# Performance work log

Measured on AMD Instinct MI355X. Metric: run time of the kernel, lower is better.

## Reference

```python
import jax, jax.numpy as jnp
import numpy as np
import math

B, S, D = 2, 2048, 1024
HQ, HKV = 16, 4
HD = D // HQ          # 64
N_REP = HQ // HKV     # 4
WINDOW = 256
ROPE_BASE = 10000.0


def _rope(x):
    # x: [b, s, h, hd]; interleaved-pair rotary (torchtune style)
    s, hd = x.shape[1], x.shape[-1]
    inv_freq = 1.0 / (ROPE_BASE ** (jnp.arange(0, hd, 2, dtype=jnp.float32) / hd))
    ang = jnp.arange(s, dtype=jnp.float32)[:, None] * inv_freq          # [s, hd/2]
    cos = jnp.cos(ang)[None, :, None, :].astype(x.dtype)
    sin = jnp.sin(ang)[None, :, None, :].astype(x.dtype)
    x1, x2 = x[..., ::2], x[..., 1::2]
    out = jnp.stack([x1 * cos - x2 * sin, x1 * sin + x2 * cos], axis=-1)
    return out.reshape(x.shape)


def setup_inputs() -> dict:
    key = jax.random.key(0)
    ks = jax.random.split(key, 5)
    sc = 0.02
    return {
        "x": jax.random.normal(ks[0], (B, S, D), dtype=jnp.float32),
        "Wq": jax.random.normal(ks[1], (D, HQ * HD), dtype=jnp.float32) * sc,
        "Wk": jax.random.normal(ks[2], (D, HKV * HD), dtype=jnp.float32) * sc,
        "Wv": jax.random.normal(ks[3], (D, HKV * HD), dtype=jnp.float32) * sc,
        "Wo": jax.random.normal(ks[4], (HQ * HD, D), dtype=jnp.float32) * sc,
    }


def reference(x, Wq, Wk, Wv, Wo):
    b, s, _ = x.shape
    xq = (x @ Wq).reshape(b, s, HQ, HD)
    xk = (x @ Wk).reshape(b, s, HKV, HD)
    xv = (x @ Wv).reshape(b, s, HKV, HD)

    xq = _rope(xq)
    xk = _rope(xk)

    # GQA: repeat kv heads to match query heads
    keys = jnp.repeat(xk, N_REP, axis=2)    # [b, s, HQ, HD]
    values = jnp.repeat(xv, N_REP, axis=2)

    scores = jnp.einsum("bqhd,bkhd->bhqk", xq, keys) / math.sqrt(HD)

    # symmetric sliding window: keep |i - j| <= WINDOW // 2
    idx = jnp.arange(s)
    mask = jnp.abs(idx[:, None] - idx[None, :]) <= (WINDOW // 2)  # [s, s]
    scores = jnp.where(mask[None, None], scores, -jnp.inf)

    attn = jax.nn.softmax(scores.astype(jnp.float32), axis=-1).astype(xq.dtype)
    ctx = jnp.einsum("bhqk,bkhd->bqhd", attn, values).reshape(b, s, HQ * HD)
    return ctx @ Wo
```

## Files before the change

### kernel.cpp

```cpp
#include <hip/hip_runtime.h>

typedef unsigned short u16;
typedef unsigned int u32;
typedef __attribute__((ext_vector_type(8))) short bfrag;
typedef __attribute__((ext_vector_type(4))) float f32x4;

#define S_LEN 2048
#define DMODEL 1024
#define NHQ 16
#define NHKV 4
#define HD 64
#define HALFW 128
#define ROWS 4096
#define QSCALE 0.1803368801111244f

__device__ __forceinline__ u16 f2b(float f) {
  u32 x = __float_as_uint(f);
  return (u16)((x + 0x7fffu + ((x >> 16) & 1u)) >> 16);
}

__device__ __forceinline__ u32 cvtpk(float lo, float hi) {
  u32 r;
  asm("v_cvt_pk_bf16_f32 %0, %1, %2" : "=v"(r) : "v"(lo), "v"(hi));
  return r;
}

__device__ __forceinline__ float fexp(float x) {
  float r;
  asm("v_exp_f32 %0, %1" : "=v"(r) : "v"(x));
  return r;
}

__global__ void prep_k(const float* __restrict__ x, const float* __restrict__ Wq,
                       const float* __restrict__ Wk, const float* __restrict__ Wv,
                       const float* __restrict__ Wo, u16* __restrict__ xb,
                       u16* __restrict__ Wcat_t, u16* __restrict__ Wo_t,
                       float2* __restrict__ csT) {
  __shared__ float tile[32][33];
  int y = blockIdx.y;
  int tid = threadIdx.y * 32 + threadIdx.x;
  if (y >= 88) {
    int i = (((y - 88) * 32 + blockIdx.x) * 256 + tid) * 4;
    float4 v = *reinterpret_cast<const float4*>(x + i);
    uint2 p;
    p.x = (u32)f2b(v.x) | ((u32)f2b(v.y) << 16);
    p.y = (u32)f2b(v.z) | ((u32)f2b(v.w) << 16);
    *reinterpret_cast<uint2*>(xb + i) = p;
    return;
  }
  if (y >= 80) {
    int idx = ((y - 80) * 32 + blockIdx.x) * 256 + tid;
    int s = idx >> 5, i = idx & 31;
    double inv = pow(10000.0, -(double)(2 * i) / 64.0);
    double ang = (double)s * inv;
    csT[idx] = make_float2((float)cos(ang), (float)sin(ang));
    return;
  }
  int k0 = blockIdx.x * 32;
  const float* src; u16* dst; int ncols, n0;
  if (y < 32)      { src = Wq; dst = Wcat_t;                       ncols = 1024; n0 = y * 32; }
  else if (y < 40) { src = Wk; dst = Wcat_t + (size_t)1024 * 1024; ncols = 256;  n0 = (y - 32) * 32; }
  else if (y < 48) { src = Wv; dst = Wcat_t + (size_t)1280 * 1024; ncols = 256;  n0 = (y - 40) * 32; }
  else             { src = Wo; dst = Wo_t;                         ncols = 1024; n0 = (y - 48) * 32; }
  int tx = threadIdx.x, ty = threadIdx.y;
#pragma unroll
  for (int j = 0; j < 4; ++j)
    tile[ty + 8 * j][tx] = src[(size_t)(k0 + ty + 8 * j) * ncols + n0 + tx];
  __syncthreads();
#pragma unroll
  for (int j = 0; j < 4; ++j)
    dst[(size_t)(n0 + ty + 8 * j) * 1024 + k0 + tx] = f2b(tile[tx][ty + 8 * j]);
}

__device__ __forceinline__ void gemm_core(const u16* __restrict__ A, const u16* __restrict__ Bt,
                                          int m0, int n0, int wave, int lane,
                                          f32x4 acc[4][2]) {
  __shared__ u16 lds_a[2 * 128 * 64];
  __shared__ u16 lds_b[2 * 64 * 64];
  int t = wave * 64 + lane;
  int g = lane >> 4, col = lane & 15;
  int wm = wave >> 1, wn = wave & 1;
  int r8 = t >> 3, slot = (t & 7) ^ (r8 & 7);
  const u16* Ab = A + (size_t)(m0 + r8) * 1024 + slot * 8;
  const u16* Bb = Bt + (size_t)(n0 + r8) * 1024 + slot * 8;
  int c7 = col & 7;
  int aoff0 = (wm * 64 + col) * 64;
  int boff0 = (wn * 32 + col) * 64;
#pragma unroll
  for (int j = 0; j < 4; ++j)
    __builtin_amdgcn_global_load_lds(
        (const __attribute__((address_space(1))) u32*)(Ab + (size_t)j * 32768),
        (__attribute__((address_space(3))) u32*)(lds_a + j * 2048 + wave * 512), 16, 0, 0);
#pragma unroll
  for (int j = 0; j < 2; ++j)
    __builtin_amdgcn_global_load_lds(
        (const __attribute__((address_space(1))) u32*)(Bb + (size_t)j * 32768),
        (__attribute__((address_space(3))) u32*)(lds_b + j * 2048 + wave * 512), 16, 0, 0);
  __syncthreads();
  for (int kt = 0; kt < 16; ++kt) {
    int cur = kt & 1;
    if (kt < 15) {
      int ko = (kt + 1) * 64;
      u16* la = lds_a + (cur ^ 1) * 8192;
      u16* lb = lds_b + (cur ^ 1) * 4096;
#pragma unroll
      for (int j = 0; j < 4; ++j)
        __builtin_amdgcn_global_load_lds(
            (const __attribute__((address_space(1))) u32*)(Ab + (size_t)j * 32768 + ko),
            (__attribute__((address_space(3))) u32*)(la + j * 2048 + wave * 512), 16, 0, 0);
#pragma unroll
      for (int j = 0; j < 2; ++j)
        __builtin_amdgcn_global_load_lds(
            (const __attribute__((address_space(1))) u32*)(Bb + (size_t)j * 32768 + ko),
            (__attribute__((address_space(3))) u32*)(lb + j * 2048 + wave * 512), 16, 0, 0);
    }
    const u16* la = lds_a + cur * 8192;
    const u16* lb = lds_b + cur * 4096;
#pragma unroll
    for (int sub = 0; sub < 2; ++sub) {
      int sa = ((sub * 4 + g) ^ c7) * 8;
      bfrag af[4], bf[2];
#pragma unroll
      for (int mi = 0; mi < 4; ++mi)
        af[mi] = *reinterpret_cast<const bfrag*>(&la[aoff0 + mi * 1024 + sa]);
#pragma unroll
      for (int ni = 0; ni < 2; ++ni)
        bf[ni] = *reinterpret_cast<const bfrag*>(&lb[boff0 + ni * 1024 + sa]);
#pragma unroll
      for (int mi = 0; mi < 4; ++mi)
#pragma unroll
        for (int ni = 0; ni < 2; ++ni)
          acc[mi][ni] = __builtin_amdgcn_mfma_f32_16x16x32_bf16(af[mi], bf[ni], acc[mi][ni], 0, 0, 0);
    }
    if (kt < 15) __syncthreads();
  }
}

__global__ __launch_bounds__(256) void gemm_qkv_k(const u16* __restrict__ A, const u16* __restrict__ Bt,
                                                  const float2* __restrict__ csT,
                                                  u16* __restrict__ Qr, u16* __restrict__ Kr,
                                                  u16* __restrict__ Vt) {
  int t = threadIdx.x;
  int wave = t >> 6, lane = t & 63;
  int g = lane >> 4, col = lane & 15;
  int m0 = blockIdx.y * 128, n0 = blockIdx.x * 64;
  int wm = wave >> 1, wn = wave & 1;
  f32x4 acc[4][2] = {};
  gemm_core(A, Bt, m0, n0, wave, lane, acc);
  bool odd = (col & 1) != 0;
#pragma unroll
  for (int mi = 0; mi < 4; ++mi)
#pragma unroll
    for (int ni = 0; ni < 2; ++ni) {
      int cg = n0 + wn * 32 + ni * 16 + col;
      int rowbase = m0 + wm * 64 + mi * 16 + g * 4;
      if (cg < 1024) {
        int hq = cg >> 6, d = cg & 63, i = d >> 1;
        u16* dst = Qr + ((size_t)((rowbase >> 11) * NHQ + hq) * S_LEN + (rowbase & 2047)) * HD + d;
#pragma unroll
        for (int r = 0; r < 4; ++r) {
          int s = (rowbase + r) & 2047;
          float v = acc[mi][ni][r];
          float pv = __shfl_xor(v, 1);
          float2 cs = csT[s * 32 + i];
          float o = odd ? (pv * cs.y + v * cs.x) : (v * cs.x - pv * cs.y);
          dst[(size_t)r * HD] = f2b(o * QSCALE);
        }
      } else if (cg < 1280) {
        int j = cg - 1024;
        int kh = j >> 6, d = j & 63, i = d >> 1;
        u16* dst = Kr + ((size_t)((rowbase >> 11) * NHKV + kh) * S_LEN + (rowbase & 2047)) * HD + d;
#pragma unroll
        for (int r = 0; r < 4; ++r) {
          int s = (rowbase + r) & 2047;
          float v = acc[mi][ni][r];
          float pv = __shfl_xor(v, 1);
          float2 cs = csT[s * 32 + i];
          float o = odd ? (pv * cs.y + v * cs.x) : (v * cs.x - pv * cs.y);
          dst[(size_t)r * HD] = f2b(o);
        }
      } else {
        int j = cg - 1280;
        int kh = j >> 6, d = j & 63;
        int b = rowbase >> 11, s0 = rowbase & 2047;
        uint2 o;
        o.x = (u32)f2b(acc[mi][ni][0]) | ((u32)f2b(acc[mi][ni][1]) << 16);
        o.y = (u32)f2b(acc[mi][ni][2]) | ((u32)f2b(acc[mi][ni][3]) << 16);
        *reinterpret_cast<uint2*>(Vt + ((size_t)(b * NHKV + kh) * HD + d) * S_LEN + s0) = o;
      }
    }
}

__global__ __launch_bounds__(256) void gemm_bt_k(const u16* __restrict__ A, const u16* __restrict__ Bt,
                                                 float* __restrict__ C, int N) {
  int t = threadIdx.x;
  int wave = t >> 6, lane = t & 63;
  int g = lane >> 4, col = lane & 15;
  int m0 = blockIdx.y * 128, n0 = blockIdx.x * 64;
  int wm = wave >> 1, wn = wave & 1;
  f32x4 acc[4][2] = {};
  gemm_core(A, Bt, m0, n0, wave, lane, acc);
#pragma unroll
  for (int mi = 0; mi < 4; ++mi)
#pragma unroll
    for (int ni = 0; ni < 2; ++ni) {
      int row = m0 + wm * 64 + mi * 16 + g * 4;
      int cc = n0 + wn * 32 + ni * 16 + col;
#pragma unroll
      for (int r = 0; r < 4; ++r)
        C[(size_t)(row + r) * N + cc] = acc[mi][ni][r];
    }
}

__global__ __launch_bounds__(256) void attn_k(const u16* __restrict__ Qr, const u16* __restrict__ Kr,
                                              const u16* __restrict__ Vt, u16* __restrict__ ctx) {
  int bid = blockIdx.x;
  int qblk = bid & 15, h = (bid >> 4) & 15, b = bid >> 8;
  int wave = threadIdx.x >> 6, lane = threadIdx.x & 63;
  int g = lane >> 4, col = lane & 15;
  int kv = h >> 2;
  int q0 = qblk * 128 + wave * 32;
  const u16* Qb = Qr + (size_t)(b * NHQ + h) * S_LEN * HD;
  const u16* Kb = Kr + (size_t)(b * NHKV + kv) * S_LEN * HD;
  const u16* Vb = Vt + (size_t)(b * NHKV + kv) * HD * S_LEN;
  bfrag qf[2][2];
#pragma unroll
  for (int qg = 0; qg < 2; ++qg) {
    qf[qg][0] = *reinterpret_cast<const bfrag*>(&Qb[(size_t)(q0 + qg * 16 + col) * HD + 8 * g]);
    qf[qg][1] = *reinterpret_cast<const bfrag*>(&Qb[(size_t)(q0 + qg * 16 + col) * HD + 32 + 8 * g]);
  }
  f32x4 octx[2][4] = {};
  float lacc[2] = {0.f, 0.f};
  int qi[2] = {q0 + col, q0 + 16 + col};
  bool hi5 = (threadIdx.x & 32) != 0;
  int l0b = (col + ((lane >> 4) & 1) * 32) << 2;
  int l1b = l0b + 64;
  int lo = q0 - HALFW; if (lo < 0) lo = 0; lo &= ~31;
  int hi = q0 + 32 + HALFW; if (hi > S_LEN) hi = S_LEN;

  auto loadK = [&](bfrag* kf, int c0) {
#pragma unroll
    for (int kt = 0; kt < 2; ++kt)
#pragma unroll
      for (int dh = 0; dh < 2; ++dh)
        kf[kt * 2 + dh] = *reinterpret_cast<const bfrag*>(
            &Kb[(size_t)(c0 + kt * 16 + col) * HD + 32 * dh + 8 * g]);
  };
  auto loadV = [&](bfrag* vf, int c0) {
#pragma unroll
    for (int n = 0; n < 4; ++n)
      vf[n] = *reinterpret_cast<const bfrag*>(&Vb[(size_t)(n * 16 + col) * S_LEN + c0 + 8 * g]);
  };
  auto compute = [&](const bfrag* kf, const bfrag* vf, int c0) {
    f32x4 s[2][2] = {};
    __builtin_amdgcn_s_setprio(1);
#pragma unroll
    for (int kt = 0; kt < 2; ++kt)
#pragma unroll
      for (int dh = 0; dh < 2; ++dh) {
        s[0][kt] = __builtin_amdgcn_mfma_f32_16x16x32_bf16(kf[kt * 2 + dh], qf[0][dh], s[0][kt], 0, 0, 0);
        s[1][kt] = __builtin_amdgcn_mfma_f32_16x16x32_bf16(kf[kt * 2 + dh], qf[1][dh], s[1][kt], 0, 0, 0);
      }
    __builtin_amdgcn_s_setprio(0);
    bool full = (c0 >= q0 + 31 - HALFW) && (c0 + 31 <= q0 + HALFW);
    union { bfrag f; u32 w[4]; } pb[2];
#pragma unroll
    for (int qg = 0; qg < 2; ++qg) {
      float p0[4], p1[4];
      if (full) {
#pragma unroll
        for (int r = 0; r < 4; ++r) { p0[r] = fexp(s[qg][0][r]); p1[r] = fexp(s[qg][1][r]); }
      } else {
        int d0 = c0 + 4 * g - qi[qg] + HALFW;
#pragma unroll
        for (int r = 0; r < 4; ++r) {
          p0[r] = ((u32)(d0 + r) <= 2u * HALFW) ? fexp(s[qg][0][r]) : 0.f;
          p1[r] = ((u32)(d0 + 16 + r) <= 2u * HALFW) ? fexp(s[qg][1][r]) : 0.f;
        }
      }
      lacc[qg] += ((p0[0] + p0[1]) + (p0[2] + p0[3])) + ((p1[0] + p1[1]) + (p1[2] + p1[3]));
      u32 pk0 = cvtpk(p0[0], p0[1]), pk1 = cvtpk(p0[2], p0[3]);
      u32 pk2 = cvtpk(p1[0], p1[1]), pk3 = cvtpk(p1[2], p1[3]);
      u32 a0 = (u32)__builtin_amdgcn_ds_bpermute(l0b, (int)pk0);
      u32 b0 = (u32)__builtin_amdgcn_ds_bpermute(l0b, (int)pk2);
      u32 a1 = (u32)__builtin_amdgcn_ds_bpermute(l0b, (int)pk1);
      u32 b1 = (u32)__builtin_amdgcn_ds_bpermute(l0b, (int)pk3);
      u32 a2 = (u32)__builtin_amdgcn_ds_bpermute(l1b, (int)pk0);
      u32 b2 = (u32)__builtin_amdgcn_ds_bpermute(l1b, (int)pk2);
      u32 a3 = (u32)__builtin_amdgcn_ds_bpermute(l1b, (int)pk1);
      u32 b3 = (u32)__builtin_amdgcn_ds_bpermute(l1b, (int)pk3);
      pb[qg].w[0] = hi5 ? b0 : a0;
      pb[qg].w[1] = hi5 ? b1 : a1;
      pb[qg].w[2] = hi5 ? b2 : a2;
      pb[qg].w[3] = hi5 ? b3 : a3;
    }
    __builtin_amdgcn_s_setprio(1);
#pragma unroll
    for (int n = 0; n < 4; ++n) {
      octx[0][n] = __builtin_amdgcn_mfma_f32_16x16x32_bf16(vf[n], pb[0].f, octx[0][n], 0, 0, 0);
      octx[1][n] = __builtin_amdgcn_mfma_f32_16x16x32_bf16(vf[n], pb[1].f, octx[1][n], 0, 0, 0);
    }
    __builtin_amdgcn_s_setprio(0);
  };

  bfrag kA[4], vA[4], kB[4], vB[4];
  loadK(kA, lo);
  loadV(vA, lo);
  for (int c0 = lo; c0 < hi; c0 += 64) {
    if (c0 + 32 < hi) { loadK(kB, c0 + 32); loadV(vB, c0 + 32); }
    compute(kA, vA, c0);
    if (c0 + 32 < hi) {
      if (c0 + 64 < hi) { loadK(kA, c0 + 64); loadV(vA, c0 + 64); }
      compute(kB, vB, c0 + 32);
    }
  }
#pragma unroll
  for (int qg = 0; qg < 2; ++qg) {
    float l = lacc[qg] + __shfl_xor(lacc[qg], 16);
    l += __shfl_xor(l, 32);
    float linv = __builtin_amdgcn_rcpf(l);
    u16* cb = ctx + (size_t)b * S_LEN * DMODEL + (size_t)(q0 + qg * 16 + col) * DMODEL + h * HD;
#pragma unroll
    for (int n = 0; n < 4; ++n) {
      uint2 o;
      o.x = cvtpk(octx[qg][n][0] * linv, octx[qg][n][1] * linv);
      o.y = cvtpk(octx[qg][n][2] * linv, octx[qg][n][3] * linv);
      *reinterpret_cast<uint2*>(cb + n * 16 + 4 * g) = o;
    }
  }
}

extern "C" void kernel_launch(void* const* d_in, const int* in_sizes, int n_in,
                              void* d_out, int out_size, void* d_ws, size_t ws_size,
                              hipStream_t stream) {
  (void)in_sizes; (void)n_in; (void)out_size; (void)ws_size;
  const float* x  = (const float*)d_in[0];
  const float* Wq = (const float*)d_in[1];
  const float* Wk = (const float*)d_in[2];
  const float* Wv = (const float*)d_in[3];
  const float* Wo = (const float*)d_in[4];
  char* ws = (char*)d_ws;
  u16*    xb     = (u16*)(ws + 0);
  u16*    Wcat_t = (u16*)(ws + 8388608);
  u16*    Wo_t   = (u16*)(ws + 11534336);
  u16*    Qr     = (u16*)(ws + 13631488);
  u16*    Kr     = (u16*)(ws + 22020096);
  u16*    Vt     = (u16*)(ws + 24117248);
  u16*    ctxb   = (u16*)(ws + 26214400);
  float2* csT    = (float2*)(ws + 34603008);

  prep_k<<<dim3(32, 216), dim3(32, 8), 0, stream>>>(x, Wq, Wk, Wv, Wo, xb, Wcat_t, Wo_t, csT);
  gemm_qkv_k<<<dim3(24, 32), 256, 0, stream>>>(xb, Wcat_t, csT, Qr, Kr, Vt);
  attn_k<<<512, 256, 0, stream>>>(Qr, Kr, Vt, ctxb);
  gemm_bt_k<<<dim3(16, 32), 256, 0, stream>>>(ctxb, Wo_t, (float*)d_out, 1024);
}
```

Baseline: 75.07 us.

## Split attention KV range across waves with LDS reduction of partial outputs

```diff
diff --git a/kernel.cpp b/kernel.cpp
--- a/kernel.cpp
+++ b/kernel.cpp
@@ -214,12 +214,13 @@
 
 __global__ __launch_bounds__(256) void attn_k(const u16* __restrict__ Qr, const u16* __restrict__ Kr,
                                               const u16* __restrict__ Vt, u16* __restrict__ ctx) {
+  __shared__ float cls[3][64][34];
   int bid = blockIdx.x;
-  int qblk = bid & 15, h = (bid >> 4) & 15, b = bid >> 8;
+  int qblk = bid & 63, h = (bid >> 6) & 15, b = bid >> 10;
   int wave = threadIdx.x >> 6, lane = threadIdx.x & 63;
   int g = lane >> 4, col = lane & 15;
   int kv = h >> 2;
-  int q0 = qblk * 128 + wave * 32;
+  int q0 = qblk * 32;
   const u16* Qb = Qr + (size_t)(b * NHQ + h) * S_LEN * HD;
   const u16* Kb = Kr + (size_t)(b * NHKV + kv) * S_LEN * HD;
   const u16* Vb = Vt + (size_t)(b * NHKV + kv) * HD * S_LEN;
@@ -304,28 +305,54 @@
   };
 
   bfrag kA[4], vA[4], kB[4], vB[4];
-  loadK(kA, lo);
-  loadV(vA, lo);
-  for (int c0 = lo; c0 < hi; c0 += 64) {
-    if (c0 + 32 < hi) { loadK(kB, c0 + 32); loadV(vB, c0 + 32); }
+  int start = lo + wave * 32;
+  if (start < hi) { loadK(kA, start); loadV(vA, start); }
+  for (int c0 = start; c0 < hi; c0 += 256) {
+    if (c0 + 128 < hi) { loadK(kB, c0 + 128); loadV(vB, c0 + 128); }
     compute(kA, vA, c0);
-    if (c0 + 32 < hi) {
-      if (c0 + 64 < hi) { loadK(kA, c0 + 64); loadV(vA, c0 + 64); }
-      compute(kB, vB, c0 + 32);
-    }
-  }
-#pragma unroll
-  for (int qg = 0; qg < 2; ++qg) {
-    float l = lacc[qg] + __shfl_xor(lacc[qg], 16);
-    l += __shfl_xor(l, 32);
-    float linv = __builtin_amdgcn_rcpf(l);
-    u16* cb = ctx + (size_t)b * S_LEN * DMODEL + (size_t)(q0 + qg * 16 + col) * DMODEL + h * HD;
-#pragma unroll
-    for (int n = 0; n < 4; ++n) {
-      uint2 o;
-      o.x = cvtpk(octx[qg][n][0] * linv, octx[qg][n][1] * linv);
-      o.y = cvtpk(octx[qg][n][2] * linv, octx[qg][n][3] * linv);
-      *reinterpret_cast<uint2*>(cb + n * 16 + 4 * g) = o;
+    if (c0 + 128 < hi) {
+      if (c0 + 256 < hi) { loadK(kA, c0 + 256); loadV(vA, c0 + 256); }
+      compute(kB, vB, c0 + 128);
+    }
+  }
+  if (wave != 0) {
+#pragma unroll
+    for (int qg = 0; qg < 2; ++qg)
+#pragma unroll
+      for (int n = 0; n < 4; ++n)
+#pragma unroll
+        for (int r = 0; r < 4; ++r)
+          cls[wave - 1][lane][qg * 16 + n * 4 + r] = octx[qg][n][r];
+    cls[wave - 1][lane][32] = lacc[0];
+    cls[wave - 1][lane][33] = lacc[1];
+  }
+  __syncthreads();
+  if (wave == 0) {
+#pragma unroll
+    for (int w = 0; w < 3; ++w) {
+#pragma unroll
+      for (int qg = 0; qg < 2; ++qg)
+#pragma unroll
+        for (int n = 0; n < 4; ++n)
+#pragma unroll
+          for (int r = 0; r < 4; ++r)
+            octx[qg][n][r] += cls[w][lane][qg * 16 + n * 4 + r];
+      lacc[0] += cls[w][lane][32];
+      lacc[1] += cls[w][lane][33];
+    }
+#pragma unroll
+    for (int qg = 0; qg < 2; ++qg) {
+      float l = lacc[qg] + __shfl_xor(lacc[qg], 16);
+      l += __shfl_xor(l, 32);
+      float linv = __builtin_amdgcn_rcpf(l);
+      u16* cb = ctx + (size_t)b * S_LEN * DMODEL + (size_t)(q0 + qg * 16 + col) * DMODEL + h * HD;
+#pragma unroll
+      for (int n = 0; n < 4; ++n) {
+        uint2 o;
+        o.x = cvtpk(octx[qg][n][0] * linv, octx[qg][n][1] * linv);
+        o.y = cvtpk(octx[qg][n][2] * linv, octx[qg][n][3] * linv);
+        *reinterpret_cast<uint2*>(cb + n * 16 + 4 * g) = o;
+      }
     }
   }
 }
@@ -351,6 +378,6 @@
 
   prep_k<<<dim3(32, 216), dim3(32, 8), 0, stream>>>(x, Wq, Wk, Wv, Wo, xb, Wcat_t, Wo_t, csT);
   gemm_qkv_k<<<dim3(24, 32), 256, 0, stream>>>(xb, Wcat_t, csT, Qr, Kr, Vt);
-  attn_k<<<512, 256, 0, stream>>>(Qr, Kr, Vt, ctxb);
+  attn_k<<<2048, 256, 0, stream>>>(Qr, Kr, Vt, ctxb);
   gemm_bt_k<<<dim3(16, 32), 256, 0, stream>>>(ctxb, Wo_t, (float*)d_out, 1024);
 }
```

New measurement: 84.39 us. 12.4% more time.
